# Kernel optimization log

Measured on AMD Instinct MI355X. Metric: run time of the kernel, lower is better.

Reference implementation:

```python
import jax, jax.numpy as jnp
import numpy as np

NUM_USERS = 25000
NUM_ITEMS = 25000
N_NODES = NUM_USERS + NUM_ITEMS
N_EDGES = 800000
EMBED_K = 64
N_LAYERS = 3
LRELU_ALPHA = 0.2  # tf.nn.leaky_relu default
EPS = 1e-12        # tf.nn.l2_normalize default epsilon


def setup_inputs() -> dict:
    key = jax.random.key(0)
    ks = jax.random.split(key, 12)
    return {
        "adj_rows": jax.random.randint(ks[0], (N_EDGES,), 0, N_NODES, dtype=jnp.int32),
        "adj_cols": jax.random.randint(ks[1], (N_EDGES,), 0, N_NODES, dtype=jnp.int32),
        "adj_vals": jax.random.uniform(ks[2], (N_EDGES,), dtype=jnp.float32),
        "Gu0": jax.random.normal(ks[3], (NUM_USERS, EMBED_K), dtype=jnp.float32) * 0.1,
        "Gi0": jax.random.normal(ks[4], (NUM_ITEMS, EMBED_K), dtype=jnp.float32) * 0.1,
        "W_gc": jax.random.normal(ks[5], (N_LAYERS, EMBED_K, EMBED_K), dtype=jnp.float32) * 0.1,
        "b_gc": jax.random.normal(ks[6], (N_LAYERS, EMBED_K), dtype=jnp.float32) * 0.1,
        "W_bi": jax.random.normal(ks[7], (N_LAYERS, EMBED_K, EMBED_K), dtype=jnp.float32) * 0.1,
        "b_bi": jax.random.normal(ks[8], (N_LAYERS, EMBED_K), dtype=jnp.float32) * 0.1,
        "user": jax.random.randint(ks[9], (4096,), 0, NUM_USERS, dtype=jnp.int32),
        "item": jax.random.randint(ks[10], (4096,), 0, NUM_ITEMS, dtype=jnp.int32),
    }


def _propagate(adj_rows, adj_cols, adj_vals, Gu0, Gi0, W_gc, b_gc, W_bi, b_bi):
    # ego: [N, d] concatenation of user + item 0th-layer embeddings
    ego = jnp.concatenate([Gu0, Gi0], axis=0)
    all_embeddings = [ego]
    for k in range(W_gc.shape[0]):
        # sparse A_hat @ ego via COO gather + segment_sum (replaces folded sparse_dense_matmul)
        side = jax.ops.segment_sum(adj_vals[:, None] * ego[adj_cols], adj_rows,
                                   num_segments=N_NODES)
        sum_emb = jax.nn.leaky_relu(side @ W_gc[k] + b_gc[k][None, :], LRELU_ALPHA)
        bi_emb = jax.nn.leaky_relu((ego * side) @ W_bi[k] + b_bi[k][None, :], LRELU_ALPHA)
        ego = sum_emb + bi_emb  # message_dropout = 0 -> identity
        norm = ego * jax.lax.rsqrt(
            jnp.maximum(jnp.sum(ego * ego, axis=1, keepdims=True), EPS))
        all_embeddings.append(norm)
        # NOTE: next layer consumes the UN-normalized ego, as in the original
    all_embeddings = jnp.concatenate(all_embeddings, axis=1)  # [N, d*(L+1)]
    gu = all_embeddings[:NUM_USERS]
    gi = all_embeddings[NUM_USERS:]
    return gu, gi


def reference(adj_rows, adj_cols, adj_vals, Gu0, Gi0, W_gc, b_gc, W_bi, b_bi, user, item):
    gu, gi = _propagate(adj_rows, adj_cols, adj_vals, Gu0, Gi0, W_gc, b_gc, W_bi, b_bi)
    # call(): embedding lookup + dot product per (user, item) pair
    gamma_u = gu[user]
    gamma_i = gi[item]
    xui = jnp.sum(gamma_u * gamma_i, axis=1)
    return xui, gu, gi
```

## Files before the change

kernel.cpp:

```cpp
#include <hip/hip_runtime.h>

#define NUM_USERS 25000
#define NUM_ITEMS 25000
#define N_NODES   50000
#define N_EDGES   800000
#define K         64
#define N_QUERY   4096
#define LRELU     0.2f

#define NBUCKET   196
#define A1_CHUNK  8192
#define A2_CHUNK  4096
#define BMAX      4608

typedef unsigned short ushort_t;
typedef unsigned long long u64_t;

__device__ __forceinline__ size_t node_out_offset(int n) {
    return (size_t)N_QUERY + (size_t)n * 256;
}

__device__ __forceinline__ ushort_t f2bf(float x) {
    unsigned u = __float_as_uint(x);
    return (ushort_t)((u + 0x7FFFu + ((u >> 16) & 1u)) >> 16);
}
__device__ __forceinline__ float bf2f(ushort_t v) {
    return __uint_as_float(((unsigned)v) << 16);
}

__global__ __launch_bounds__(256) void init_kernel(
    const float* __restrict__ Gu0, const float* __restrict__ Gi0,
    const float* __restrict__ W_gc, const float* __restrict__ W_bi,
    ushort_t* __restrict__ egb, float* __restrict__ WT, float* __restrict__ out)
{
    int tid = blockIdx.x * 256 + threadIdx.x;
    if (tid < N_NODES * K) {
        int n = tid >> 6;
        int d = tid & 63;
        float v = (n < NUM_USERS) ? Gu0[tid] : Gi0[tid - NUM_USERS * K];
        egb[tid] = f2bf(v);
        out[node_out_offset(n) + d] = v;
    } else {
        int tw = tid - N_NODES * K;
        if (tw < 3 * 2 * 64 * 64) {
            int k   = tw >> 13;
            int m   = (tw >> 12) & 1;
            int idx = tw & 4095;
            int o   = idx >> 6;
            int j   = idx & 63;
            const float* src = m ? W_bi : W_gc;
            WT[tw] = src[k * 4096 + j * 64 + o];
        }
    }
}

__global__ __launch_bounds__(256) void bhist_kernel(
    const int* __restrict__ rows, int* __restrict__ bucket_count)
{
    __shared__ int h[NBUCKET];
    int t = threadIdx.x;
    if (t < NBUCKET) h[t] = 0;
    __syncthreads();
    int base = blockIdx.x * A1_CHUNK;
    for (int i = t; i < A1_CHUNK; i += 256) {
        int e = base + i;
        if (e < N_EDGES) atomicAdd(&h[rows[e] >> 8], 1);
    }
    __syncthreads();
    if (t < NBUCKET) atomicAdd(&bucket_count[t], h[t]);
}

__global__ __launch_bounds__(256) void bscan_kernel(
    const int* __restrict__ bucket_count,
    int* __restrict__ gbase, int* __restrict__ cursor)
{
    __shared__ int sh[256];
    int t = threadIdx.x;
    sh[t] = (t < NBUCKET) ? bucket_count[t] : 0;
    __syncthreads();
    for (int off = 1; off < 256; off <<= 1) {
        int v = (t >= off) ? sh[t - off] : 0;
        __syncthreads();
        sh[t] += v;
        __syncthreads();
    }
    int excl = (t == 0) ? 0 : sh[t - 1];
    if (t < NBUCKET) { gbase[t] = excl; cursor[t] = excl; }
    if (t == NBUCKET) gbase[NBUCKET] = N_EDGES;
}

__global__ __launch_bounds__(256) void bscatter_kernel(
    const int* __restrict__ rows, const int* __restrict__ cols,
    const float* __restrict__ vals, int* __restrict__ cursor,
    u64_t* __restrict__ csr64)
{
    __shared__ u64_t recs[A2_CHUNK];
    __shared__ int hist[NBUCKET], lbase[NBUCKET], lcur[NBUCKET];
    int t = threadIdx.x;
    if (t < NBUCKET) { hist[t] = 0; lcur[t] = 0; }
    __syncthreads();
    int base = blockIdx.x * A2_CHUNK;
    for (int i = t; i < A2_CHUNK; i += 256) {
        int e = base + i;
        if (e < N_EDGES) {
            int r = rows[e];
            u64_t rec = ((u64_t)(unsigned)__float_as_uint(vals[e]) << 32)
                      | ((u64_t)(unsigned)cols[e] << 16)
                      | (unsigned)r;
            recs[i] = rec;
            atomicAdd(&hist[r >> 8], 1);
        }
    }
    __syncthreads();
    if (t < NBUCKET) lbase[t] = atomicAdd(&cursor[t], hist[t]);
    __syncthreads();
    for (int i = t; i < A2_CHUNK; i += 256) {
        int e = base + i;
        if (e < N_EDGES) {
            u64_t rec = recs[i];
            int b = (int)((rec >> 8) & 0xFF);
            int dst = lbase[b] + atomicAdd(&lcur[b], 1);
            csr64[dst] = rec;
        }
    }
}

__global__ __launch_bounds__(256) void bsort_kernel(
    const int* __restrict__ gbase, u64_t* __restrict__ csr64,
    int* __restrict__ offs)
{
    __shared__ u64_t recs[BMAX];
    __shared__ int hist[256], lscan[256], lcur[256];
    int b = blockIdx.x, t = threadIdx.x;
    int g0 = gbase[b];
    int nb = gbase[b + 1] - g0;
    if (nb > BMAX) nb = BMAX;
    hist[t] = 0; lcur[t] = 0;
    __syncthreads();
    for (int i = t; i < nb; i += 256) {
        u64_t rec = csr64[g0 + i];
        recs[i] = rec;
        atomicAdd(&hist[(int)(rec & 0xFF)], 1);
    }
    __syncthreads();
    int v0 = hist[t];
    lscan[t] = v0;
    __syncthreads();
    for (int off = 1; off < 256; off <<= 1) {
        int v = (t >= off) ? lscan[t - off] : 0;
        __syncthreads();
        lscan[t] += v;
        __syncthreads();
    }
    int excl = lscan[t] - v0;
    int row = (b << 8) + t;
    if (row < N_NODES) offs[row] = g0 + excl;
    if (b == 0 && t == 0) offs[N_NODES] = N_EDGES;
    __syncthreads();
    lscan[t] = excl;
    __syncthreads();
    for (int i = t; i < nb; i += 256) {
        u64_t rec = recs[i];
        int rl = (int)(rec & 0xFF);
        int pos = lscan[rl] + atomicAdd(&lcur[rl], 1);
        u64_t outrec = (rec >> 32 << 32) | ((rec >> 16) & 0xFFFFu);
        csr64[g0 + pos] = outrec;
    }
}

__global__ __launch_bounds__(512, 8) void gather_kernel(
    const int* __restrict__ offs, const long long* __restrict__ csr_cv,
    const unsigned* __restrict__ egb2, float* __restrict__ side)
{
    int t = threadIdx.x;
    int wave = t >> 6;
    int lane = t & 63;
    int par  = lane >> 5;
    int d2   = lane & 31;
    int node = blockIdx.x * 8 + wave;

    int beg = offs[node];
    int end = offs[node + 1];
    float a0 = 0.f, a1 = 0.f;
    int j = beg;

    for (; j + 16 <= end; j += 16) {
        long long cv[8];
        #pragma unroll
        for (int u = 0; u < 8; ++u)
            cv[u] = __builtin_nontemporal_load(csr_cv + j + 2 * u + par);
        unsigned g[8];
        #pragma unroll
        for (int u = 0; u < 8; ++u)
            g[u] = egb2[((size_t)(unsigned)(cv[u] & 0xffffffffLL) << 5) + d2];
        #pragma unroll
        for (int u = 0; u < 8; ++u) {
            float v = __uint_as_float((unsigned)((u64_t)cv[u] >> 32));
            a0 = fmaf(v, bf2f((ushort_t)(g[u] & 0xFFFFu)), a0);
            a1 = fmaf(v, bf2f((ushort_t)(g[u] >> 16)), a1);
        }
    }

    if (j < end) {
        long long cv[8];
        bool ok[8];
        #pragma unroll
        for (int u = 0; u < 8; ++u) {
            int idx = j + 2 * u + par;
            ok[u] = idx < end;
            int idxc = ok[u] ? idx : (end - 1);
            cv[u] = __builtin_nontemporal_load(csr_cv + idxc);
        }
        unsigned g[8];
        #pragma unroll
        for (int u = 0; u < 8; ++u)
            g[u] = egb2[((size_t)(unsigned)(cv[u] & 0xffffffffLL) << 5) + d2];
        #pragma unroll
        for (int u = 0; u < 8; ++u) {
            float v = ok[u] ? __uint_as_float((unsigned)((u64_t)cv[u] >> 32)) : 0.f;
            a0 = fmaf(v, bf2f((ushort_t)(g[u] & 0xFFFFu)), a0);
            a1 = fmaf(v, bf2f((ushort_t)(g[u] >> 16)), a1);
        }
    }

    a0 += __shfl_xor(a0, 32);
    a1 += __shfl_xor(a1, 32);
    if (par == 0)
        *(float2*)(side + ((size_t)node << 6) + 2 * d2) = make_float2(a0, a1);
}

__global__ __launch_bounds__(256, 2) void transform_kernel(
    const float* __restrict__ side, ushort_t* __restrict__ egb,
    const float* __restrict__ WgT, const float* __restrict__ WbT,
    const float* __restrict__ bgc, const float* __restrict__ bbi,
    float* __restrict__ out, int layer_k)
{
    __shared__ float s_s [64 * 64];
    __shared__ float s_es[64 * 64];
    __shared__ float s_wg[64 * 64];
    __shared__ float s_wb[64 * 64];

    int t = threadIdx.x;
    int base = blockIdx.x * 64;

    for (int idx = t; idx < 64 * 16; idx += 256) {
        int r = idx >> 4;
        int q = idx & 15;
        int qs = q ^ ((r >> 2) & 7);
        float4 sv = make_float4(0.f, 0.f, 0.f, 0.f);
        float4 ev = make_float4(0.f, 0.f, 0.f, 0.f);
        int node = base + r;
        if (node < N_NODES) {
            sv = *(const float4*)(side + ((size_t)node << 6) + 4 * q);
            ushort4 uv = *(const ushort4*)(egb + ((size_t)node << 6) + 4 * q);
            ev = make_float4(bf2f(uv.x), bf2f(uv.y), bf2f(uv.z), bf2f(uv.w));
        }
        *(float4*)&s_s [r * 64 + 4 * qs] = sv;
        *(float4*)&s_es[r * 64 + 4 * qs] =
            make_float4(ev.x * sv.x, ev.y * sv.y, ev.z * sv.z, ev.w * sv.w);
        *(float4*)&s_wg[r * 64 + 4 * qs] = *(const float4*)(WgT + (size_t)r * 64 + 4 * q);
        *(float4*)&s_wb[r * 64 + 4 * qs] = *(const float4*)(WbT + (size_t)r * 64 + 4 * q);
    }
    __syncthreads();

    const int o0  = (t & 15) << 2;
    const int ln0 = (t >> 4) << 2;
    const int sa  = (t >> 4) & 7;
    const int sw  = t & 7;

    float accg[4][4] = {};
    float accb[4][4] = {};

    #pragma unroll 4
    for (int kq = 0; kq < 16; ++kq) {
        const int qa = (kq ^ sa) << 2;
        const int qw = (kq ^ sw) << 2;
        float4 a[4], b[4], wg[4], wb[4];
        #pragma unroll
        for (int i = 0; i < 4; ++i) {
            a[i] = *(const float4*)&s_s [(ln0 + i) * 64 + qa];
            b[i] = *(const float4*)&s_es[(ln0 + i) * 64 + qa];
        }
        #pragma unroll
        for (int j = 0; j < 4; ++j) {
            wg[j] = *(const float4*)&s_wg[(o0 + j) * 64 + qw];
            wb[j] = *(const float4*)&s_wb[(o0 + j) * 64 + qw];
        }
        #pragma unroll
        for (int i = 0; i < 4; ++i) {
            #pragma unroll
            for (int j = 0; j < 4; ++j) {
                accg[i][j] = fmaf(a[i].x, wg[j].x, accg[i][j]);
                accg[i][j] = fmaf(a[i].y, wg[j].y, accg[i][j]);
                accg[i][j] = fmaf(a[i].z, wg[j].z, accg[i][j]);
                accg[i][j] = fmaf(a[i].w, wg[j].w, accg[i][j]);
                accb[i][j] = fmaf(b[i].x, wb[j].x, accb[i][j]);
                accb[i][j] = fmaf(b[i].y, wb[j].y, accb[i][j]);
                accb[i][j] = fmaf(b[i].z, wb[j].z, accb[i][j]);
                accb[i][j] = fmaf(b[i].w, wb[j].w, accb[i][j]);
            }
        }
    }

    float4 bg4 = *(const float4*)(bgc + o0);
    float4 bb4 = *(const float4*)(bbi + o0);
    float bgv[4] = {bg4.x, bg4.y, bg4.z, bg4.w};
    float bbv[4] = {bb4.x, bb4.y, bb4.z, bb4.w};

    #pragma unroll
    for (int i = 0; i < 4; ++i) {
        int node = base + ln0 + i;
        float en[4];
        float ss = 0.f;
        #pragma unroll
        for (int j = 0; j < 4; ++j) {
            float g = accg[i][j] + bgv[j];
            float h = accb[i][j] + bbv[j];
            g = (g > 0.f) ? g : LRELU * g;
            h = (h > 0.f) ? h : LRELU * h;
            en[j] = g + h;
            ss = fmaf(en[j], en[j], ss);
        }
        #pragma unroll
        for (int m = 1; m < 16; m <<= 1) ss += __shfl_xor(ss, m);
        float inv = rsqrtf(fmaxf(ss, 1e-12f));
        if (node < N_NODES) {
            if (layer_k != 2)
                *(ushort4*)(egb + ((size_t)node << 6) + o0) =
                    make_ushort4(f2bf(en[0]), f2bf(en[1]), f2bf(en[2]), f2bf(en[3]));
            *(float4*)(out + node_out_offset(node) + (size_t)(layer_k + 1) * K + o0) =
                make_float4(en[0] * inv, en[1] * inv, en[2] * inv, en[3] * inv);
        }
    }
}

__global__ __launch_bounds__(256) void xui_kernel(
    const int* __restrict__ user, const int* __restrict__ item,
    float* __restrict__ out)
{
    int idx = blockIdx.x * 4 + (threadIdx.x >> 6);
    if (idx >= N_QUERY) return;
    int lane = threadIdx.x & 63;
    int u  = user[idx];
    int it = item[idx];
    const float4* gu = (const float4*)(out + (size_t)N_QUERY + (size_t)u * 256);
    const float4* gi = (const float4*)(out + (size_t)N_QUERY + (size_t)NUM_USERS * 256
                                           + (size_t)it * 256);
    float4 a = gu[lane];
    float4 b = gi[lane];
    float d = a.x * b.x + a.y * b.y + a.z * b.z + a.w * b.w;
    #pragma unroll
    for (int off = 32; off; off >>= 1) d += __shfl_xor(d, off);
    if (lane == 0) out[idx] = d;
}

extern "C" void kernel_launch(void* const* d_in, const int* in_sizes, int n_in,
                              void* d_out, int out_size, void* d_ws, size_t ws_size,
                              hipStream_t stream)
{
    const int*   adj_rows = (const int*)  d_in[0];
    const int*   adj_cols = (const int*)  d_in[1];
    const float* adj_vals = (const float*)d_in[2];
    const float* Gu0      = (const float*)d_in[3];
    const float* Gi0      = (const float*)d_in[4];
    const float* W_gc     = (const float*)d_in[5];
    const float* b_gc     = (const float*)d_in[6];
    const float* W_bi     = (const float*)d_in[7];
    const float* b_bi     = (const float*)d_in[8];
    const int*   user     = (const int*)  d_in[9];
    const int*   item     = (const int*)  d_in[10];

    float* out = (float*)d_out;

    float*    side   = (float*)d_ws;
    ushort_t* egb    = (ushort_t*)(side + (size_t)N_NODES * K);
    u64_t*    csr64  = (u64_t*)(egb + (size_t)N_NODES * K);
    int*      offs   = (int*)(csr64 + N_EDGES);
    int*      gbase  = offs + N_NODES + 1;
    int*      cursor = gbase + NBUCKET + 1;
    int*      bcnt   = cursor + NBUCKET;
    float*    WT     = (float*)(bcnt + NBUCKET);

    hipMemsetAsync(bcnt, 0, NBUCKET * sizeof(int), stream);
    bhist_kernel<<<(N_EDGES + A1_CHUNK - 1) / A1_CHUNK, 256, 0, stream>>>(adj_rows, bcnt);
    bscan_kernel<<<1, 256, 0, stream>>>(bcnt, gbase, cursor);
    bscatter_kernel<<<(N_EDGES + A2_CHUNK - 1) / A2_CHUNK, 256, 0, stream>>>(
        adj_rows, adj_cols, adj_vals, cursor, csr64);
    bsort_kernel<<<NBUCKET, 256, 0, stream>>>(gbase, csr64, offs);

    {
        int total = N_NODES * K + 3 * 2 * 64 * 64;
        init_kernel<<<(total + 255) / 256, 256, 0, stream>>>(
            Gu0, Gi0, W_gc, W_bi, egb, WT, out);
    }

    for (int k = 0; k < 3; ++k) {
        gather_kernel<<<N_NODES / 8, 512, 0, stream>>>(
            offs, (const long long*)csr64, (const unsigned*)egb, side);
        transform_kernel<<<(N_NODES + 63) / 64, 256, 0, stream>>>(
            side, egb,
            WT + (size_t)k * 8192, WT + (size_t)k * 8192 + 4096,
            b_gc + (size_t)k * K, b_bi + (size_t)k * K,
            out, k);
    }

    xui_kernel<<<N_QUERY / 4, 256, 0, stream>>>(user, item, out);
}
```

Baseline: 244.0 us.

## Fuse sparse gather with dense transform per layer and merge init with histogram

Each layer now runs one kernel. It gathers neighbour sums for 64 nodes straight into shared memory and then applies the two 64x64 transforms, so the fp32 side buffer no longer makes a round trip through global memory. Embeddings are ping-ponged between two bf16 buffers to avoid a read/write race across blocks. The init kernel and the bucket histogram are also merged into one launch. In exchange, the fused kernel uses 512 threads with lower occupancy, and gather parallelism per block drops to 8 waves handling 8 nodes each serially, which may hurt latency hiding.

```diff
diff --git a/kernel.cpp b/kernel.cpp
--- a/kernel.cpp
+++ b/kernel.cpp
@@ -10,6 +10,7 @@
 
 #define NBUCKET   196
 #define A1_CHUNK  8192
+#define NHBLK     ((N_EDGES + A1_CHUNK - 1) / A1_CHUNK)
 #define A2_CHUNK  4096
 #define BMAX      4608
 
@@ -28,46 +29,46 @@
     return __uint_as_float(((unsigned)v) << 16);
 }
 
-__global__ __launch_bounds__(256) void init_kernel(
+__global__ __launch_bounds__(256) void init_hist_kernel(
     const float* __restrict__ Gu0, const float* __restrict__ Gi0,
     const float* __restrict__ W_gc, const float* __restrict__ W_bi,
-    ushort_t* __restrict__ egb, float* __restrict__ WT, float* __restrict__ out)
-{
-    int tid = blockIdx.x * 256 + threadIdx.x;
-    if (tid < N_NODES * K) {
-        int n = tid >> 6;
-        int d = tid & 63;
-        float v = (n < NUM_USERS) ? Gu0[tid] : Gi0[tid - NUM_USERS * K];
-        egb[tid] = f2bf(v);
-        out[node_out_offset(n) + d] = v;
+    const int* __restrict__ rows,
+    ushort_t* __restrict__ egb, float* __restrict__ WT, float* __restrict__ out,
+    int* __restrict__ bucket_count)
+{
+    __shared__ int h[NBUCKET];
+    int b = blockIdx.x, t = threadIdx.x;
+    if (b < NHBLK) {
+        if (t < NBUCKET) h[t] = 0;
+        __syncthreads();
+        int base = b * A1_CHUNK;
+        for (int i = t; i < A1_CHUNK; i += 256) {
+            int e = base + i;
+            if (e < N_EDGES) atomicAdd(&h[rows[e] >> 8], 1);
+        }
+        __syncthreads();
+        if (t < NBUCKET) atomicAdd(&bucket_count[t], h[t]);
     } else {
-        int tw = tid - N_NODES * K;
-        if (tw < 3 * 2 * 64 * 64) {
-            int k   = tw >> 13;
-            int m   = (tw >> 12) & 1;
-            int idx = tw & 4095;
-            int o   = idx >> 6;
-            int j   = idx & 63;
-            const float* src = m ? W_bi : W_gc;
-            WT[tw] = src[k * 4096 + j * 64 + o];
-        }
-    }
-}
-
-__global__ __launch_bounds__(256) void bhist_kernel(
-    const int* __restrict__ rows, int* __restrict__ bucket_count)
-{
-    __shared__ int h[NBUCKET];
-    int t = threadIdx.x;
-    if (t < NBUCKET) h[t] = 0;
-    __syncthreads();
-    int base = blockIdx.x * A1_CHUNK;
-    for (int i = t; i < A1_CHUNK; i += 256) {
-        int e = base + i;
-        if (e < N_EDGES) atomicAdd(&h[rows[e] >> 8], 1);
-    }
-    __syncthreads();
-    if (t < NBUCKET) atomicAdd(&bucket_count[t], h[t]);
+        int tid = (b - NHBLK) * 256 + t;
+        if (tid < N_NODES * K) {
+            int n = tid >> 6;
+            int d = tid & 63;
+            float v = (n < NUM_USERS) ? Gu0[tid] : Gi0[tid - NUM_USERS * K];
+            egb[tid] = f2bf(v);
+            out[node_out_offset(n) + d] = v;
+        } else {
+            int tw = tid - N_NODES * K;
+            if (tw < 3 * 2 * 64 * 64) {
+                int k   = tw >> 13;
+                int m   = (tw >> 12) & 1;
+                int idx = tw & 4095;
+                int o   = idx >> 6;
+                int j   = idx & 63;
+                const float* src = m ? W_bi : W_gc;
+                WT[tw] = src[k * 4096 + j * 64 + o];
+            }
+        }
+    }
 }
 
 __global__ __launch_bounds__(256) void bscan_kernel(
@@ -168,118 +169,114 @@
     }
 }
 
-__global__ __launch_bounds__(512, 8) void gather_kernel(
+__global__ __launch_bounds__(512, 4) void layer_kernel(
     const int* __restrict__ offs, const long long* __restrict__ csr_cv,
-    const unsigned* __restrict__ egb2, float* __restrict__ side)
-{
-    int t = threadIdx.x;
-    int wave = t >> 6;
-    int lane = t & 63;
-    int par  = lane >> 5;
-    int d2   = lane & 31;
-    int node = blockIdx.x * 8 + wave;
-
-    int beg = offs[node];
-    int end = offs[node + 1];
-    float a0 = 0.f, a1 = 0.f;
-    int j = beg;
-
-    for (; j + 16 <= end; j += 16) {
-        long long cv[8];
-        #pragma unroll
-        for (int u = 0; u < 8; ++u)
-            cv[u] = __builtin_nontemporal_load(csr_cv + j + 2 * u + par);
-        unsigned g[8];
-        #pragma unroll
-        for (int u = 0; u < 8; ++u)
-            g[u] = egb2[((size_t)(unsigned)(cv[u] & 0xffffffffLL) << 5) + d2];
-        #pragma unroll
-        for (int u = 0; u < 8; ++u) {
-            float v = __uint_as_float((unsigned)((u64_t)cv[u] >> 32));
-            a0 = fmaf(v, bf2f((ushort_t)(g[u] & 0xFFFFu)), a0);
-            a1 = fmaf(v, bf2f((ushort_t)(g[u] >> 16)), a1);
-        }
-    }
-
-    if (j < end) {
-        long long cv[8];
-        bool ok[8];
-        #pragma unroll
-        for (int u = 0; u < 8; ++u) {
-            int idx = j + 2 * u + par;
-            ok[u] = idx < end;
-            int idxc = ok[u] ? idx : (end - 1);
-            cv[u] = __builtin_nontemporal_load(csr_cv + idxc);
-        }
-        unsigned g[8];
-        #pragma unroll
-        for (int u = 0; u < 8; ++u)
-            g[u] = egb2[((size_t)(unsigned)(cv[u] & 0xffffffffLL) << 5) + d2];
-        #pragma unroll
-        for (int u = 0; u < 8; ++u) {
-            float v = ok[u] ? __uint_as_float((unsigned)((u64_t)cv[u] >> 32)) : 0.f;
-            a0 = fmaf(v, bf2f((ushort_t)(g[u] & 0xFFFFu)), a0);
-            a1 = fmaf(v, bf2f((ushort_t)(g[u] >> 16)), a1);
-        }
-    }
-
-    a0 += __shfl_xor(a0, 32);
-    a1 += __shfl_xor(a1, 32);
-    if (par == 0)
-        *(float2*)(side + ((size_t)node << 6) + 2 * d2) = make_float2(a0, a1);
-}
-
-__global__ __launch_bounds__(256, 2) void transform_kernel(
-    const float* __restrict__ side, ushort_t* __restrict__ egb,
+    const ushort_t* __restrict__ egb_in, ushort_t* __restrict__ egb_out,
     const float* __restrict__ WgT, const float* __restrict__ WbT,
     const float* __restrict__ bgc, const float* __restrict__ bbi,
     float* __restrict__ out, int layer_k)
 {
-    __shared__ float s_s [64 * 64];
-    __shared__ float s_es[64 * 64];
-    __shared__ float s_wg[64 * 64];
-    __shared__ float s_wb[64 * 64];
+    __shared__ float    s_side[64 * 64];
+    __shared__ ushort_t s_eg  [64 * 64];
+    __shared__ float    s_wg  [64 * 64];
+    __shared__ float    s_wb  [64 * 64];
 
     int t = threadIdx.x;
     int base = blockIdx.x * 64;
-
-    for (int idx = t; idx < 64 * 16; idx += 256) {
-        int r = idx >> 4;
-        int q = idx & 15;
+    const unsigned* egb2 = (const unsigned*)egb_in;
+
+    for (int i = t; i < 64 * 16; i += 512) {
+        int r = i >> 4, q = i & 15;
         int qs = q ^ ((r >> 2) & 7);
-        float4 sv = make_float4(0.f, 0.f, 0.f, 0.f);
-        float4 ev = make_float4(0.f, 0.f, 0.f, 0.f);
+        *(float4*)&s_wg[r * 64 + 4 * qs] = *(const float4*)(WgT + r * 64 + 4 * q);
+        *(float4*)&s_wb[r * 64 + 4 * qs] = *(const float4*)(WbT + r * 64 + 4 * q);
         int node = base + r;
+        ushort4 uv = make_ushort4(0, 0, 0, 0);
+        if (node < N_NODES)
+            uv = *(const ushort4*)(egb_in + ((size_t)node << 6) + 4 * q);
+        *(ushort4*)&s_eg[r * 64 + 4 * qs] = uv;
+    }
+
+    int wave = t >> 6, lane = t & 63;
+    int par  = lane >> 5;
+    int d2   = lane & 31;
+
+    for (int nn = 0; nn < 8; ++nn) {
+        int r = wave * 8 + nn;
+        int node = base + r;
+        float a0 = 0.f, a1 = 0.f;
         if (node < N_NODES) {
-            sv = *(const float4*)(side + ((size_t)node << 6) + 4 * q);
-            ushort4 uv = *(const ushort4*)(egb + ((size_t)node << 6) + 4 * q);
-            ev = make_float4(bf2f(uv.x), bf2f(uv.y), bf2f(uv.z), bf2f(uv.w));
-        }
-        *(float4*)&s_s [r * 64 + 4 * qs] = sv;
-        *(float4*)&s_es[r * 64 + 4 * qs] =
-            make_float4(ev.x * sv.x, ev.y * sv.y, ev.z * sv.z, ev.w * sv.w);
-        *(float4*)&s_wg[r * 64 + 4 * qs] = *(const float4*)(WgT + (size_t)r * 64 + 4 * q);
-        *(float4*)&s_wb[r * 64 + 4 * qs] = *(const float4*)(WbT + (size_t)r * 64 + 4 * q);
+            int beg = offs[node];
+            int end = offs[node + 1];
+            int j = beg;
+            for (; j + 16 <= end; j += 16) {
+                long long cv[8];
+                #pragma unroll
+                for (int u = 0; u < 8; ++u)
+                    cv[u] = __builtin_nontemporal_load(csr_cv + j + 2 * u + par);
+                unsigned g[8];
+                #pragma unroll
+                for (int u = 0; u < 8; ++u)
+                    g[u] = egb2[((size_t)(unsigned)(cv[u] & 0xffffffffLL) << 5) + d2];
+                #pragma unroll
+                for (int u = 0; u < 8; ++u) {
+                    float v = __uint_as_float((unsigned)((u64_t)cv[u] >> 32));
+                    a0 = fmaf(v, bf2f((ushort_t)(g[u] & 0xFFFFu)), a0);
+                    a1 = fmaf(v, bf2f((ushort_t)(g[u] >> 16)), a1);
+                }
+            }
+            if (j < end) {
+                long long cv[8];
+                bool ok[8];
+                #pragma unroll
+                for (int u = 0; u < 8; ++u) {
+                    int idx = j + 2 * u + par;
+                    ok[u] = idx < end;
+                    int idxc = ok[u] ? idx : (end - 1);
+                    cv[u] = __builtin_nontemporal_load(csr_cv + idxc);
+                }
+                unsigned g[8];
+                #pragma unroll
+                for (int u = 0; u < 8; ++u)
+                    g[u] = egb2[((size_t)(unsigned)(cv[u] & 0xffffffffLL) << 5) + d2];
+                #pragma unroll
+                for (int u = 0; u < 8; ++u) {
+                    float v = ok[u] ? __uint_as_float((unsigned)((u64_t)cv[u] >> 32)) : 0.f;
+                    a0 = fmaf(v, bf2f((ushort_t)(g[u] & 0xFFFFu)), a0);
+                    a1 = fmaf(v, bf2f((ushort_t)(g[u] >> 16)), a1);
+                }
+            }
+        }
+        a0 += __shfl_xor(a0, 32);
+        a1 += __shfl_xor(a1, 32);
+        if (par == 0) {
+            int q  = d2 >> 1;
+            int qs = q ^ ((r >> 2) & 7);
+            *(float2*)&s_side[r * 64 + (qs << 2) + ((d2 & 1) << 1)] =
+                make_float2(a0, a1);
+        }
     }
     __syncthreads();
 
     const int o0  = (t & 15) << 2;
-    const int ln0 = (t >> 4) << 2;
-    const int sa  = (t >> 4) & 7;
+    const int ln0 = (t >> 4) << 1;
+    const int sa  = (ln0 >> 2) & 7;
     const int sw  = t & 7;
 
-    float accg[4][4] = {};
-    float accb[4][4] = {};
+    float accg[2][4] = {};
+    float accb[2][4] = {};
 
     #pragma unroll 4
     for (int kq = 0; kq < 16; ++kq) {
         const int qa = (kq ^ sa) << 2;
         const int qw = (kq ^ sw) << 2;
-        float4 a[4], b[4], wg[4], wb[4];
+        float4 a[2], es[2], wg[4], wb[4];
         #pragma unroll
-        for (int i = 0; i < 4; ++i) {
-            a[i] = *(const float4*)&s_s [(ln0 + i) * 64 + qa];
-            b[i] = *(const float4*)&s_es[(ln0 + i) * 64 + qa];
+        for (int i = 0; i < 2; ++i) {
+            a[i] = *(const float4*)&s_side[(ln0 + i) * 64 + qa];
+            ushort4 ue = *(const ushort4*)&s_eg[(ln0 + i) * 64 + qa];
+            es[i] = make_float4(bf2f(ue.x) * a[i].x, bf2f(ue.y) * a[i].y,
+                                bf2f(ue.z) * a[i].z, bf2f(ue.w) * a[i].w);
         }
         #pragma unroll
         for (int j = 0; j < 4; ++j) {
@@ -287,17 +284,17 @@
             wb[j] = *(const float4*)&s_wb[(o0 + j) * 64 + qw];
         }
         #pragma unroll
-        for (int i = 0; i < 4; ++i) {
+        for (int i = 0; i < 2; ++i) {
             #pragma unroll
             for (int j = 0; j < 4; ++j) {
-                accg[i][j] = fmaf(a[i].x, wg[j].x, accg[i][j]);
-                accg[i][j] = fmaf(a[i].y, wg[j].y, accg[i][j]);
-                accg[i][j] = fmaf(a[i].z, wg[j].z, accg[i][j]);
-                accg[i][j] = fmaf(a[i].w, wg[j].w, accg[i][j]);
-                accb[i][j] = fmaf(b[i].x, wb[j].x, accb[i][j]);
-                accb[i][j] = fmaf(b[i].y, wb[j].y, accb[i][j]);
-                accb[i][j] = fmaf(b[i].z, wb[j].z, accb[i][j]);
-                accb[i][j] = fmaf(b[i].w, wb[j].w, accb[i][j]);
+                accg[i][j] = fmaf(a[i].x,  wg[j].x, accg[i][j]);
+                accg[i][j] = fmaf(a[i].y,  wg[j].y, accg[i][j]);
+                accg[i][j] = fmaf(a[i].z,  wg[j].z, accg[i][j]);
+                accg[i][j] = fmaf(a[i].w,  wg[j].w, accg[i][j]);
+                accb[i][j] = fmaf(es[i].x, wb[j].x, accb[i][j]);
+                accb[i][j] = fmaf(es[i].y, wb[j].y, accb[i][j]);
+                accb[i][j] = fmaf(es[i].z, wb[j].z, accb[i][j]);
+                accb[i][j] = fmaf(es[i].w, wb[j].w, accb[i][j]);
             }
         }
     }
@@ -308,7 +305,7 @@
     float bbv[4] = {bb4.x, bb4.y, bb4.z, bb4.w};
 
     #pragma unroll
-    for (int i = 0; i < 4; ++i) {
+    for (int i = 0; i < 2; ++i) {
         int node = base + ln0 + i;
         float en[4];
         float ss = 0.f;
@@ -326,7 +323,7 @@
         float inv = rsqrtf(fmaxf(ss, 1e-12f));
         if (node < N_NODES) {
             if (layer_k != 2)
-                *(ushort4*)(egb + ((size_t)node << 6) + o0) =
+                *(ushort4*)(egb_out + ((size_t)node << 6) + o0) =
                     make_ushort4(f2bf(en[0]), f2bf(en[1]), f2bf(en[2]), f2bf(en[3]));
             *(float4*)(out + node_out_offset(node) + (size_t)(layer_k + 1) * K + o0) =
                 make_float4(en[0] * inv, en[1] * inv, en[2] * inv, en[3] * inv);
@@ -372,9 +369,9 @@
 
     float* out = (float*)d_out;
 
-    float*    side   = (float*)d_ws;
-    ushort_t* egb    = (ushort_t*)(side + (size_t)N_NODES * K);
-    u64_t*    csr64  = (u64_t*)(egb + (size_t)N_NODES * K);
+    ushort_t* egbA   = (ushort_t*)d_ws;
+    ushort_t* egbB   = egbA + (size_t)N_NODES * K;
+    u64_t*    csr64  = (u64_t*)(egbB + (size_t)N_NODES * K);
     int*      offs   = (int*)(csr64 + N_EDGES);
     int*      gbase  = offs + N_NODES + 1;
     int*      cursor = gbase + NBUCKET + 1;
@@ -382,26 +379,25 @@
     float*    WT     = (float*)(bcnt + NBUCKET);
 
     hipMemsetAsync(bcnt, 0, NBUCKET * sizeof(int), stream);
-    bhist_kernel<<<(N_EDGES + A1_CHUNK - 1) / A1_CHUNK, 256, 0, stream>>>(adj_rows, bcnt);
+    {
+        int init_blocks = (N_NODES * K + 3 * 2 * 64 * 64 + 255) / 256;
+        init_hist_kernel<<<NHBLK + init_blocks, 256, 0, stream>>>(
+            Gu0, Gi0, W_gc, W_bi, adj_rows, egbA, WT, out, bcnt);
+    }
     bscan_kernel<<<1, 256, 0, stream>>>(bcnt, gbase, cursor);
     bscatter_kernel<<<(N_EDGES + A2_CHUNK - 1) / A2_CHUNK, 256, 0, stream>>>(
         adj_rows, adj_cols, adj_vals, cursor, csr64);
     bsort_kernel<<<NBUCKET, 256, 0, stream>>>(gbase, csr64, offs);
 
-    {
-        int total = N_NODES * K + 3 * 2 * 64 * 64;
-        init_kernel<<<(total + 255) / 256, 256, 0, stream>>>(
-            Gu0, Gi0, W_gc, W_bi, egb, WT, out);
-    }
-
+    ushort_t* ein  = egbA;
+    ushort_t* eout = egbB;
     for (int k = 0; k < 3; ++k) {
-        gather_kernel<<<N_NODES / 8, 512, 0, stream>>>(
-            offs, (const long long*)csr64, (const unsigned*)egb, side);
-        transform_kernel<<<(N_NODES + 63) / 64, 256, 0, stream>>>(
-            side, egb,
+        layer_kernel<<<(N_NODES + 63) / 64, 512, 0, stream>>>(
+            offs, (const long long*)csr64, ein, eout,
             WT + (size_t)k * 8192, WT + (size_t)k * 8192 + 4096,
             b_gc + (size_t)k * K, b_bi + (size_t)k * K,
             out, k);
+        ushort_t* tmp = ein; ein = eout; eout = tmp;
     }
 
     xui_kernel<<<N_QUERY / 4, 256, 0, stream>>>(user, item, out);
```

New measurement: 253.7 us. 4.0% more time.
